# Optimization experiments

Hardware: AMD Instinct MI355X
Metric: run time of the kernel (lower is better)

## Reference

```python
import jax, jax.numpy as jnp
import numpy as np

B, S_SRC, S_TGT, H, C = 32, 128, 129, 512, 32000


def setup_inputs() -> dict:
    key = jax.random.key(0)
    ks = jax.random.split(key, 16)
    sc = 0.02
    return {
        "source": jax.random.randint(ks[0], (B, S_SRC), 0, C),
        "target": jax.random.randint(ks[1], (B, S_TGT), 0, C),
        "embed": jax.random.normal(ks[2], (C, H), jnp.float32) * sc,
        "enc_Wih": jax.random.normal(ks[3], (H, H), jnp.float32) * sc,
        "enc_Whh": jax.random.normal(ks[4], (H, H), jnp.float32) * sc,
        "enc_bih": jnp.zeros((H,), jnp.float32),
        "enc_bhh": jnp.zeros((H,), jnp.float32),
        "dec_Wih": jax.random.normal(ks[5], (H, H), jnp.float32) * sc,
        "dec_Whh": jax.random.normal(ks[6], (H, H), jnp.float32) * sc,
        "dec_bih": jnp.zeros((H,), jnp.float32),
        "dec_bhh": jnp.zeros((H,), jnp.float32),
        "attn_W": jax.random.normal(ks[7], (H, H), jnp.float32) * sc,
        "attn_b": jnp.zeros((H,), jnp.float32),
        "out_W": jax.random.normal(ks[8], (C, 2 * H), jnp.float32) * sc,
        "out_b": jnp.zeros((C,), jnp.float32),
    }


def _rnn(xs, h0, Wih, Whh, bih, bhh):
    # xs: [T, B, H], h0: [B, H]; Elman RNN with tanh (torch nn.RNN default)
    def step(h, x):
        h = jnp.tanh(x @ Wih.T + bih + h @ Whh.T + bhh)
        return h, h
    _, ys = jax.lax.scan(step, h0, xs)
    return ys  # [T, B, H]


def reference(source, target, embed, enc_Wih, enc_Whh, enc_bih, enc_bhh,
              dec_Wih, dec_Whh, dec_bih, dec_bhh, attn_W, attn_b, out_W, out_b):
    dec_input = target[:, :-1]                       # [B, T]
    enc_emb = embed[source].transpose(1, 0, 2)       # [S, B, H]
    dec_emb = embed[dec_input].transpose(1, 0, 2)    # [T, B, H]

    h0 = jnp.zeros((source.shape[0], embed.shape[1]), embed.dtype)
    enc_outputs = _rnn(enc_emb, h0, enc_Wih, enc_Whh, enc_bih, enc_bhh)  # [S, B, H]

    enc_bsh = enc_outputs.transpose(1, 0, 2)                  # [B, S, H]
    enc_t = enc_bsh @ attn_W.T + attn_b                       # [B, S, H] (attn linear)

    def dec_step(h, x):
        h = jnp.tanh(x @ dec_Wih.T + dec_bih + h @ dec_Whh.T + dec_bhh)  # [B, H]
        score = jnp.einsum('bh,bsh->bs', h, enc_t)            # [B, S]
        attn = jax.nn.softmax(score, axis=-1)                 # [B, S]
        ctx = jnp.einsum('bs,bsh->bh', attn, enc_bsh)         # [B, H]
        return h, (jnp.concatenate([h, ctx], axis=-1), attn)

    h_enc = enc_outputs[-1]                                   # [B, H]
    _, (model_hidden, attn_all) = jax.lax.scan(dec_step, h_enc, dec_emb)
    # model_hidden: [T, B, 2H], attn_all: [T, B, S]

    logits = model_hidden @ out_W.T + out_b                   # [T, B, C]
    output_logit = logits.transpose(1, 0, 2)                  # [B, T, C]
    att_weight = attn_all.transpose(1, 2, 0)                  # [B, S, T] = trained_attn.transpose(2,1)
    return output_logit, att_weight
```

## Files before the change

### kernel.cpp

```cpp
#include <hip/hip_runtime.h>
#include <hip/hip_bf16.h>
#include <stdint.h>

typedef unsigned short u16;
typedef __bf16 bf16x8 __attribute__((ext_vector_type(8)));
typedef float f32x4 __attribute__((ext_vector_type(4)));

__device__ __forceinline__ u16 f2bf(float f) {
  uint32_t u = __float_as_uint(f);
  u = (u + 0x7FFFu + ((u >> 16) & 1u)) >> 16;
  return (u16)u;
}

__device__ __forceinline__ void gl2lds16(const void* g, void* l) {
  __builtin_amdgcn_global_load_lds(
      (const __attribute__((address_space(1))) void*)g,
      (__attribute__((address_space(3))) void*)l, 16, 0, 0);
}

__global__ void cvt_bf16_arr(const float* __restrict__ in, u16* __restrict__ out, int n4) {
  int i = blockIdx.x * blockDim.x + threadIdx.x;
  if (i >= n4) return;
  float4 v = ((const float4*)in)[i];
  ushort4 o;
  o.x = f2bf(v.x); o.y = f2bf(v.y); o.z = f2bf(v.z); o.w = f2bf(v.w);
  ((ushort4*)out)[i] = o;
}

__global__ void pack_whh(const float* __restrict__ W, uint32_t* __restrict__ out) {
  int idx = blockIdx.x * 256 + threadIdx.x;
  int p = idx >> 9, j = idx & 511;
  float a = W[j * 512 + 2 * p];
  float b = W[j * 512 + 2 * p + 1];
  out[p * 512 + j] = (uint32_t)f2bf(a) | ((uint32_t)f2bf(b) << 16);
}

__global__ void gather_embed(const int* __restrict__ tok, const float* __restrict__ embed,
                             u16* __restrict__ out, int tokStride) {
  int m = blockIdx.x;
  int t = threadIdx.x;
  int token = tok[(m >> 7) * tokStride + (m & 127)];
  float4 v = ((const float4*)(embed + (long)token * 512))[t];
  ushort4 o;
  o.x = f2bf(v.x); o.y = f2bf(v.y); o.z = f2bf(v.z); o.w = f2bf(v.w);
  ((ushort4*)(out + (long)m * 512))[t] = o;
}

__global__ __launch_bounds__(256) void gemm_bf16_kernel(
    const u16* __restrict__ A, const u16* __restrict__ B,
    const float* __restrict__ bias, float* __restrict__ C,
    int M, int N, int K) {
  __shared__ __align__(16) u16 As[4096];
  __shared__ __align__(16) u16 Bs[4096];
  const int tid = threadIdx.x;
  const int lane = tid & 63;
  const int wv = tid >> 6;
  const int wr = wv >> 1, wc = wv & 1;
  const long m0 = (long)blockIdx.y * 128;
  const long n0 = (long)blockIdx.x * 128;

  f32x4 zero = {0.f, 0.f, 0.f, 0.f};
  f32x4 acc[4][4];
#pragma unroll
  for (int i = 0; i < 4; ++i)
#pragma unroll
    for (int j = 0; j < 4; ++j) acc[i][j] = zero;

  const u16* Ag = A + (m0 + (tid >> 2)) * (long)K + (tid & 3) * 8;
  const u16* Bg = B + (n0 + (tid >> 2)) * (long)K + (tid & 3) * 8;
  const u16* Ag2 = Ag + 64 * (long)K;
  const u16* Bg2 = Bg + 64 * (long)K;
  u16* AsW = As + (tid >> 6) * 512;
  u16* BsW = Bs + (tid >> 6) * 512;
  const int ra = (wr * 64 + (lane & 15)) * 32 + (lane >> 4) * 8;
  const int rb = (wc * 64 + (lane & 15)) * 32 + (lane >> 4) * 8;

  for (int kt = 0; kt < K; kt += 32) {
    __syncthreads();
    gl2lds16(Ag + kt, AsW);
    gl2lds16(Ag2 + kt, AsW + 2048);
    gl2lds16(Bg + kt, BsW);
    gl2lds16(Bg2 + kt, BsW + 2048);
    __syncthreads();
    bf16x8 af[4], bfr[4];
#pragma unroll
    for (int i = 0; i < 4; ++i) af[i] = *(const bf16x8*)&As[ra + i * 512];
#pragma unroll
    for (int j = 0; j < 4; ++j) bfr[j] = *(const bf16x8*)&Bs[rb + j * 512];
#pragma unroll
    for (int i = 0; i < 4; ++i)
#pragma unroll
      for (int j = 0; j < 4; ++j)
        acc[i][j] = __builtin_amdgcn_mfma_f32_16x16x32_bf16(af[i], bfr[j], acc[i][j], 0, 0, 0);
  }

#pragma unroll
  for (int i = 0; i < 4; ++i) {
    const long row = m0 + wr * 64 + i * 16 + ((lane >> 4) << 2);
#pragma unroll
    for (int j = 0; j < 4; ++j) {
      const long col = n0 + wc * 64 + j * 16 + (lane & 15);
      const float bv = bias ? bias[col] : 0.f;
#pragma unroll
      for (int r = 0; r < 4; ++r)
        C[(row + r) * (long)N + col] = acc[i][j][r] + bv;
    }
  }
}

__global__ __launch_bounds__(1024) void enc_rnn(
    const float* __restrict__ pre, const uint32_t* __restrict__ WhhP,
    const float* __restrict__ bih, const float* __restrict__ bhh,
    float* __restrict__ enc_bsh, u16* __restrict__ enc_bf) {
  const int b = blockIdx.x, tid = threadIdx.x;
  const int j = tid & 511, half = tid >> 9;
  __shared__ float h_sh[512];
  __shared__ float part[2][512];
  if (tid < 512) h_sh[tid] = 0.f;
  const float biasj = bih[j] + bhh[j];
  const uint32_t* wp = WhhP + (long)half * 128 * 512 + j;
  const float2* hp = (const float2*)&h_sh[half * 256];
  __syncthreads();
  for (int t = 0; t < 128; ++t) {
    float a0 = 0.f, a1 = 0.f;
#pragma unroll 8
    for (int kk = 0; kk < 128; kk += 2) {
      uint32_t w0 = wp[(long)kk * 512];
      uint32_t w1 = wp[(long)(kk + 1) * 512];
      float2 h0 = hp[kk];
      float2 h1 = hp[kk + 1];
      a0 += h0.x * __uint_as_float(w0 << 16) + h0.y * __uint_as_float(w0 & 0xFFFF0000u);
      a1 += h1.x * __uint_as_float(w1 << 16) + h1.y * __uint_as_float(w1 & 0xFFFF0000u);
    }
    part[half][j] = a0 + a1;
    __syncthreads();
    if (tid < 512) {
      float v = pre[((long)b * 128 + t) * 512 + j] + biasj + part[0][j] + part[1][j];
      float h = tanhf(v);
      h_sh[j] = h;
      enc_bsh[((long)b * 128 + t) * 512 + j] = h;
      enc_bf[((long)b * 128 + t) * 512 + j] = f2bf(h);
    }
    __syncthreads();
  }
}

__global__ __launch_bounds__(1024) void dec_rnn(
    const float* __restrict__ pre, const uint32_t* __restrict__ WhhP,
    const float* __restrict__ bih, const float* __restrict__ bhh,
    const float* __restrict__ enc_t, const float* __restrict__ enc_bsh,
    u16* __restrict__ Hcat, float* __restrict__ att_out) {
  const int b = blockIdx.x, tid = threadIdx.x;
  const int j = tid & 511, half = tid >> 9;
  const int lane = tid & 63, wv = tid >> 6;
  __shared__ float h_sh[512];
  __shared__ float part[2][512];
  __shared__ float sc_sh[128];
  __shared__ float at_sh[128];
  if (tid < 512) h_sh[tid] = enc_bsh[((long)b * 128 + 127) * 512 + tid];
  const float biasj = bih[j] + bhh[j];
  const uint32_t* wp = WhhP + (long)half * 128 * 512 + j;
  const float2* hp = (const float2*)&h_sh[half * 256];
  const float* et_b = enc_t + (long)b * 128 * 512;
  const float* eb_b = enc_bsh + (long)b * 128 * 512;
  __syncthreads();
  for (int t = 0; t < 128; ++t) {
    float a0 = 0.f, a1 = 0.f;
#pragma unroll 8
    for (int kk = 0; kk < 128; kk += 2) {
      uint32_t w0 = wp[(long)kk * 512];
      uint32_t w1 = wp[(long)(kk + 1) * 512];
      float2 h0 = hp[kk];
      float2 h1 = hp[kk + 1];
      a0 += h0.x * __uint_as_float(w0 << 16) + h0.y * __uint_as_float(w0 & 0xFFFF0000u);
      a1 += h1.x * __uint_as_float(w1 << 16) + h1.y * __uint_as_float(w1 & 0xFFFF0000u);
    }
    part[half][j] = a0 + a1;
    __syncthreads();
    float hreg = 0.f;
    if (tid < 512) {
      float v = pre[((long)b * 128 + t) * 512 + j] + biasj + part[0][j] + part[1][j];
      hreg = tanhf(v);
      h_sh[j] = hreg;
    }
    __syncthreads();
#pragma unroll
    for (int q = 0; q < 8; ++q) {
      int s = wv * 8 + q;
      const float* row = et_b + (long)s * 512;
      float a = 0.f;
#pragma unroll
      for (int i = 0; i < 8; ++i) a += h_sh[lane + i * 64] * row[lane + i * 64];
#pragma unroll
      for (int off = 32; off; off >>= 1) a += __shfl_xor(a, off, 64);
      if (lane == 0) sc_sh[s] = a;
    }
    __syncthreads();
    if (tid < 64) {
      float s0 = sc_sh[tid], s1 = sc_sh[tid + 64];
      float mx = fmaxf(s0, s1);
#pragma unroll
      for (int off = 32; off; off >>= 1) mx = fmaxf(mx, __shfl_xor(mx, off, 64));
      float e0 = __expf(s0 - mx), e1 = __expf(s1 - mx);
      float sm = e0 + e1;
#pragma unroll
      for (int off = 32; off; off >>= 1) sm += __shfl_xor(sm, off, 64);
      float inv = 1.f / sm;
      at_sh[tid] = e0 * inv;
      at_sh[tid + 64] = e1 * inv;
    }
    __syncthreads();
    if (tid < 128) att_out[(long)b * 16384 + (long)tid * 128 + t] = at_sh[tid];
    float cacc = 0.f;
#pragma unroll 4
    for (int si = 0; si < 64; ++si) {
      int s = half * 64 + si;
      cacc += at_sh[s] * eb_b[(long)s * 512 + j];
    }
    __syncthreads();
    part[half][j] = cacc;
    __syncthreads();
    if (tid < 512) {
      float ctx = part[0][j] + part[1][j];
      long r = ((long)b * 128 + t) * 1024;
      Hcat[r + j] = f2bf(hreg);
      Hcat[r + 512 + j] = f2bf(ctx);
    }
    __syncthreads();
  }
}

extern "C" void kernel_launch(void* const* d_in, const int* in_sizes, int n_in,
                              void* d_out, int out_size, void* d_ws, size_t ws_size,
                              hipStream_t stream) {
  (void)in_sizes; (void)n_in; (void)out_size; (void)ws_size;
  const int*   source = (const int*)d_in[0];
  const int*   target = (const int*)d_in[1];
  const float* embed  = (const float*)d_in[2];
  const float* encWih = (const float*)d_in[3];
  const float* encWhh = (const float*)d_in[4];
  const float* encBih = (const float*)d_in[5];
  const float* encBhh = (const float*)d_in[6];
  const float* decWih = (const float*)d_in[7];
  const float* decWhh = (const float*)d_in[8];
  const float* decBih = (const float*)d_in[9];
  const float* decBhh = (const float*)d_in[10];
  const float* attnW  = (const float*)d_in[11];
  const float* attnB  = (const float*)d_in[12];
  const float* outW   = (const float*)d_in[13];
  const float* outB   = (const float*)d_in[14];

  float* out_logits = (float*)d_out;
  float* out_att = out_logits + (long)32 * 128 * 32000;

  char* wsb = (char*)d_ws;
  size_t off = 0;
  auto alloc = [&](size_t bytes) {
    char* p = wsb + off;
    off += (bytes + 255) & ~(size_t)255;
    return p;
  };
  u16*      encA   = (u16*)alloc(4096l * 512 * 2);
  u16*      decA   = (u16*)alloc(4096l * 512 * 2);
  u16*      wihE   = (u16*)alloc(512l * 512 * 2);
  u16*      wihD   = (u16*)alloc(512l * 512 * 2);
  u16*      attnWb = (u16*)alloc(512l * 512 * 2);
  uint32_t* whhPe  = (uint32_t*)alloc(256l * 512 * 4);
  uint32_t* whhPd  = (uint32_t*)alloc(256l * 512 * 4);
  u16*      outWb  = (u16*)alloc(32000l * 1024 * 2);
  float*    preE   = (float*)alloc(4096l * 512 * 4);
  float*    preD   = (float*)alloc(4096l * 512 * 4);
  float*    encBsh = (float*)alloc(4096l * 512 * 4);
  u16*      encBf  = (u16*)alloc(4096l * 512 * 2);
  float*    encT   = (float*)alloc(4096l * 512 * 4);
  u16*      hcat   = (u16*)alloc(4096l * 1024 * 2);

  cvt_bf16_arr<<<256, 256, 0, stream>>>(encWih, wihE, 65536);
  cvt_bf16_arr<<<256, 256, 0, stream>>>(decWih, wihD, 65536);
  cvt_bf16_arr<<<256, 256, 0, stream>>>(attnW, attnWb, 65536);
  cvt_bf16_arr<<<32000, 256, 0, stream>>>(outW, outWb, 8192000);
  pack_whh<<<512, 256, 0, stream>>>(encWhh, whhPe);
  pack_whh<<<512, 256, 0, stream>>>(decWhh, whhPd);
  gather_embed<<<4096, 128, 0, stream>>>(source, embed, encA, 128);
  gather_embed<<<4096, 128, 0, stream>>>(target, embed, decA, 129);
  gemm_bf16_kernel<<<dim3(4, 32), 256, 0, stream>>>(encA, wihE, (const float*)nullptr, preE, 4096, 512, 512);
  gemm_bf16_kernel<<<dim3(4, 32), 256, 0, stream>>>(decA, wihD, (const float*)nullptr, preD, 4096, 512, 512);
  enc_rnn<<<32, 1024, 0, stream>>>(preE, whhPe, encBih, encBhh, encBsh, encBf);
  gemm_bf16_kernel<<<dim3(4, 32), 256, 0, stream>>>(encBf, attnWb, attnB, encT, 4096, 512, 512);
  dec_rnn<<<32, 1024, 0, stream>>>(preD, whhPd, decBih, decBhh, encT, encBsh, hcat, out_att);
  gemm_bf16_kernel<<<dim3(250, 32), 256, 0, stream>>>(hcat, outWb, outB, out_logits, 4096, 32000, 1024);
}
```

Measured before the change: 3.177 ms.

## Hoist decoder attention out of the recurrence and keep recurrent weights on-chip

The decoder's attention (scores, softmax, context) does not feed back into the hidden state, so it moves out of the sequential loop into a separate kernel. That kernel processes all 128 timesteps in parallel across a (batch, time-block) grid. A shared rnn_core kernel now serves both encoder and decoder with 512 threads. Each thread keeps 192 packed bf16 weight words in registers and the remaining 64 in LDS, instead of re-reading Whh from global memory every step, and the two-half partial-sum reduction is gone. The risks are register spilling from the large per-thread weight array, and attention now being computed from bf16-rounded hidden states.

```diff
diff --git a/kernel.cpp b/kernel.cpp
--- a/kernel.cpp
+++ b/kernel.cpp
@@ -11,6 +11,11 @@
   u = (u + 0x7FFFu + ((u >> 16) & 1u)) >> 16;
   return (u16)u;
 }
+__device__ __forceinline__ float bf2f(u16 x) {
+  return __uint_as_float(((uint32_t)x) << 16);
+}
+__device__ __forceinline__ float blo(uint32_t w) { return __uint_as_float(w << 16); }
+__device__ __forceinline__ float bhi(uint32_t w) { return __uint_as_float(w & 0xFFFF0000u); }
 
 __device__ __forceinline__ void gl2lds16(const void* g, void* l) {
   __builtin_amdgcn_global_load_lds(
@@ -108,126 +113,120 @@
   }
 }
 
-__global__ __launch_bounds__(1024) void enc_rnn(
-    const float* __restrict__ pre, const uint32_t* __restrict__ WhhP,
+__global__ __launch_bounds__(512, 2) void rnn_core(
+    const float* __restrict__ pre,
+    const uint32_t* __restrict__ WhhP,
     const float* __restrict__ bih, const float* __restrict__ bhh,
-    float* __restrict__ enc_bsh, u16* __restrict__ enc_bf) {
-  const int b = blockIdx.x, tid = threadIdx.x;
-  const int j = tid & 511, half = tid >> 9;
-  __shared__ float h_sh[512];
-  __shared__ float part[2][512];
-  if (tid < 512) h_sh[tid] = 0.f;
+    const float* __restrict__ h0,
+    float* __restrict__ hOutF, long ldF,
+    u16* __restrict__ hOutB, long ldB_,
+    float* __restrict__ hLast)
+{
+  const int b = blockIdx.x, j = threadIdx.x;
+  __shared__ __align__(16) float h_sh[512];
+  __shared__ uint32_t wlds[64][512];
+  uint32_t wreg[192];
+#pragma unroll
+  for (int r = 0; r < 192; ++r) wreg[r] = WhhP[(long)r * 512 + j];
+#pragma unroll
+  for (int p = 0; p < 64; ++p) wlds[p][j] = WhhP[(long)(192 + p) * 512 + j];
   const float biasj = bih[j] + bhh[j];
-  const uint32_t* wp = WhhP + (long)half * 128 * 512 + j;
-  const float2* hp = (const float2*)&h_sh[half * 256];
+  h_sh[j] = h0 ? h0[(long)b * 512 + j] : 0.f;
+  const float* preB = pre + (long)b * 128 * 512 + j;
   __syncthreads();
+
   for (int t = 0; t < 128; ++t) {
-    float a0 = 0.f, a1 = 0.f;
-#pragma unroll 8
-    for (int kk = 0; kk < 128; kk += 2) {
-      uint32_t w0 = wp[(long)kk * 512];
-      uint32_t w1 = wp[(long)(kk + 1) * 512];
-      float2 h0 = hp[kk];
-      float2 h1 = hp[kk + 1];
-      a0 += h0.x * __uint_as_float(w0 << 16) + h0.y * __uint_as_float(w0 & 0xFFFF0000u);
-      a1 += h1.x * __uint_as_float(w1 << 16) + h1.y * __uint_as_float(w1 & 0xFFFF0000u);
+    const float4* H4 = (const float4*)h_sh;
+    float a0 = 0.f, a1 = 0.f, a2 = 0.f, a3 = 0.f;
+#pragma unroll
+    for (int g = 0; g < 48; ++g) {
+      float4 ha = H4[2 * g];
+      float4 hb = H4[2 * g + 1];
+      uint32_t w0 = wreg[4 * g], w1 = wreg[4 * g + 1];
+      uint32_t w2 = wreg[4 * g + 2], w3 = wreg[4 * g + 3];
+      a0 += ha.x * blo(w0) + ha.y * bhi(w0);
+      a1 += ha.z * blo(w1) + ha.w * bhi(w1);
+      a2 += hb.x * blo(w2) + hb.y * bhi(w2);
+      a3 += hb.z * blo(w3) + hb.w * bhi(w3);
     }
-    part[half][j] = a0 + a1;
-    __syncthreads();
-    if (tid < 512) {
-      float v = pre[((long)b * 128 + t) * 512 + j] + biasj + part[0][j] + part[1][j];
-      float h = tanhf(v);
-      h_sh[j] = h;
-      enc_bsh[((long)b * 128 + t) * 512 + j] = h;
-      enc_bf[((long)b * 128 + t) * 512 + j] = f2bf(h);
+#pragma unroll
+    for (int g = 0; g < 16; ++g) {
+      float4 ha = H4[96 + 2 * g];
+      float4 hb = H4[96 + 2 * g + 1];
+      uint32_t w0 = wlds[4 * g][j], w1 = wlds[4 * g + 1][j];
+      uint32_t w2 = wlds[4 * g + 2][j], w3 = wlds[4 * g + 3][j];
+      a0 += ha.x * blo(w0) + ha.y * bhi(w0);
+      a1 += ha.z * blo(w1) + ha.w * bhi(w1);
+      a2 += hb.x * blo(w2) + hb.y * bhi(w2);
+      a3 += hb.z * blo(w3) + hb.w * bhi(w3);
     }
-    __syncthreads();
-  }
-}
-
-__global__ __launch_bounds__(1024) void dec_rnn(
-    const float* __restrict__ pre, const uint32_t* __restrict__ WhhP,
-    const float* __restrict__ bih, const float* __restrict__ bhh,
-    const float* __restrict__ enc_t, const float* __restrict__ enc_bsh,
-    u16* __restrict__ Hcat, float* __restrict__ att_out) {
-  const int b = blockIdx.x, tid = threadIdx.x;
-  const int j = tid & 511, half = tid >> 9;
-  const int lane = tid & 63, wv = tid >> 6;
-  __shared__ float h_sh[512];
-  __shared__ float part[2][512];
-  __shared__ float sc_sh[128];
-  __shared__ float at_sh[128];
-  if (tid < 512) h_sh[tid] = enc_bsh[((long)b * 128 + 127) * 512 + tid];
-  const float biasj = bih[j] + bhh[j];
-  const uint32_t* wp = WhhP + (long)half * 128 * 512 + j;
-  const float2* hp = (const float2*)&h_sh[half * 256];
-  const float* et_b = enc_t + (long)b * 128 * 512;
-  const float* eb_b = enc_bsh + (long)b * 128 * 512;
+    float h = tanhf(preB[(long)t * 512] + biasj + ((a0 + a1) + (a2 + a3)));
+    __syncthreads();
+    h_sh[j] = h;
+    if (hOutF) hOutF[((long)b * 128 + t) * ldF + j] = h;
+    hOutB[((long)b * 128 + t) * ldB_ + j] = f2bf(h);
+    if (hLast && t == 127) hLast[(long)b * 512 + j] = h;
+    __syncthreads();
+  }
+}
+
+__global__ __launch_bounds__(1024) void attn_fused(
+    const u16* __restrict__ hcat,
+    const float* __restrict__ encT,
+    const float* __restrict__ encBsh,
+    u16* __restrict__ hcatW,
+    float* __restrict__ attOut)
+{
+  const int b = blockIdx.x;
+  const int w = threadIdx.x >> 6, lane = threadIdx.x & 63;
+  const int t = blockIdx.y * 16 + w;
+  __shared__ float at[16][128];
+
+  float hreg[8];
+  const u16* hrow = hcat + ((long)b * 128 + t) * 1024;
+#pragma unroll
+  for (int i = 0; i < 8; ++i) hreg[i] = bf2f(hrow[lane + i * 64]);
+
+  const float* et = encT + (long)b * 128 * 512;
+  for (int s = 0; s < 128; ++s) {
+    const float* row = et + (long)s * 512;
+    float a = 0.f;
+#pragma unroll
+    for (int i = 0; i < 8; ++i) a += hreg[i] * row[lane + i * 64];
+#pragma unroll
+    for (int o = 32; o; o >>= 1) a += __shfl_xor(a, o, 64);
+    if (lane == 0) at[w][s] = a;
+  }
   __syncthreads();
-  for (int t = 0; t < 128; ++t) {
-    float a0 = 0.f, a1 = 0.f;
-#pragma unroll 8
-    for (int kk = 0; kk < 128; kk += 2) {
-      uint32_t w0 = wp[(long)kk * 512];
-      uint32_t w1 = wp[(long)(kk + 1) * 512];
-      float2 h0 = hp[kk];
-      float2 h1 = hp[kk + 1];
-      a0 += h0.x * __uint_as_float(w0 << 16) + h0.y * __uint_as_float(w0 & 0xFFFF0000u);
-      a1 += h1.x * __uint_as_float(w1 << 16) + h1.y * __uint_as_float(w1 & 0xFFFF0000u);
-    }
-    part[half][j] = a0 + a1;
-    __syncthreads();
-    float hreg = 0.f;
-    if (tid < 512) {
-      float v = pre[((long)b * 128 + t) * 512 + j] + biasj + part[0][j] + part[1][j];
-      hreg = tanhf(v);
-      h_sh[j] = hreg;
-    }
-    __syncthreads();
-#pragma unroll
-    for (int q = 0; q < 8; ++q) {
-      int s = wv * 8 + q;
-      const float* row = et_b + (long)s * 512;
-      float a = 0.f;
-#pragma unroll
-      for (int i = 0; i < 8; ++i) a += h_sh[lane + i * 64] * row[lane + i * 64];
-#pragma unroll
-      for (int off = 32; off; off >>= 1) a += __shfl_xor(a, off, 64);
-      if (lane == 0) sc_sh[s] = a;
-    }
-    __syncthreads();
-    if (tid < 64) {
-      float s0 = sc_sh[tid], s1 = sc_sh[tid + 64];
-      float mx = fmaxf(s0, s1);
-#pragma unroll
-      for (int off = 32; off; off >>= 1) mx = fmaxf(mx, __shfl_xor(mx, off, 64));
-      float e0 = __expf(s0 - mx), e1 = __expf(s1 - mx);
-      float sm = e0 + e1;
-#pragma unroll
-      for (int off = 32; off; off >>= 1) sm += __shfl_xor(sm, off, 64);
-      float inv = 1.f / sm;
-      at_sh[tid] = e0 * inv;
-      at_sh[tid + 64] = e1 * inv;
-    }
-    __syncthreads();
-    if (tid < 128) att_out[(long)b * 16384 + (long)tid * 128 + t] = at_sh[tid];
-    float cacc = 0.f;
-#pragma unroll 4
-    for (int si = 0; si < 64; ++si) {
-      int s = half * 64 + si;
-      cacc += at_sh[s] * eb_b[(long)s * 512 + j];
-    }
-    __syncthreads();
-    part[half][j] = cacc;
-    __syncthreads();
-    if (tid < 512) {
-      float ctx = part[0][j] + part[1][j];
-      long r = ((long)b * 128 + t) * 1024;
-      Hcat[r + j] = f2bf(hreg);
-      Hcat[r + 512 + j] = f2bf(ctx);
-    }
-    __syncthreads();
-  }
+
+  float s0 = at[w][lane], s1 = at[w][lane + 64];
+  float mx = fmaxf(s0, s1);
+#pragma unroll
+  for (int o = 32; o; o >>= 1) mx = fmaxf(mx, __shfl_xor(mx, o, 64));
+  float e0 = __expf(s0 - mx), e1 = __expf(s1 - mx);
+  float sm = e0 + e1;
+#pragma unroll
+  for (int o = 32; o; o >>= 1) sm += __shfl_xor(sm, o, 64);
+  float inv = 1.f / sm;
+  e0 *= inv; e1 *= inv;
+  at[w][lane] = e0;
+  at[w][lane + 64] = e1;
+  __syncthreads();
+
+  attOut[(long)b * 16384 + (long)lane * 128 + t] = e0;
+  attOut[(long)b * 16384 + (long)(lane + 64) * 128 + t] = e1;
+
+  float acc[8] = {0.f, 0.f, 0.f, 0.f, 0.f, 0.f, 0.f, 0.f};
+  const float* eb = encBsh + (long)b * 128 * 512;
+  for (int s = 0; s < 128; ++s) {
+    float ws = at[w][s];
+    const float* row = eb + (long)s * 512;
+#pragma unroll
+    for (int i = 0; i < 8; ++i) acc[i] += ws * row[lane + i * 64];
+  }
+  u16* crow = hcatW + ((long)b * 128 + t) * 1024 + 512;
+#pragma unroll
+  for (int i = 0; i < 8; ++i) crow[lane + i * 64] = f2bf(acc[i]);
 }
 
 extern "C" void kernel_launch(void* const* d_in, const int* in_sizes, int n_in,
@@ -273,6 +272,7 @@
   float*    encBsh = (float*)alloc(4096l * 512 * 4);
   u16*      encBf  = (u16*)alloc(4096l * 512 * 2);
   float*    encT   = (float*)alloc(4096l * 512 * 4);
+  float*    hlast  = (float*)alloc(32l * 512 * 4);
   u16*      hcat   = (u16*)alloc(4096l * 1024 * 2);
 
   cvt_bf16_arr<<<256, 256, 0, stream>>>(encWih, wihE, 65536);
@@ -285,8 +285,11 @@
   gather_embed<<<4096, 128, 0, stream>>>(target, embed, decA, 129);
   gemm_bf16_kernel<<<dim3(4, 32), 256, 0, stream>>>(encA, wihE, (const float*)nullptr, preE, 4096, 512, 512);
   gemm_bf16_kernel<<<dim3(4, 32), 256, 0, stream>>>(decA, wihD, (const float*)nullptr, preD, 4096, 512, 512);
-  enc_rnn<<<32, 1024, 0, stream>>>(preE, whhPe, encBih, encBhh, encBsh, encBf);
+  rnn_core<<<32, 512, 0, stream>>>(preE, whhPe, encBih, encBhh,
+      (const float*)nullptr, encBsh, 512, encBf, 512, hlast);
   gemm_bf16_kernel<<<dim3(4, 32), 256, 0, stream>>>(encBf, attnWb, attnB, encT, 4096, 512, 512);
-  dec_rnn<<<32, 1024, 0, stream>>>(preD, whhPd, decBih, decBhh, encT, encBsh, hcat, out_att);
+  rnn_core<<<32, 512, 0, stream>>>(preD, whhPd, decBih, decBhh,
+      hlast, (float*)nullptr, 512, hcat, 1024, (float*)nullptr);
+  attn_fused<<<dim3(32, 8), 1024, 0, stream>>>(hcat, encT, encBsh, hcat, out_att);
   gemm_bf16_kernel<<<dim3(250, 32), 256, 0, stream>>>(hcat, outWb, outB, out_logits, 4096, 32000, 1024);
 }
```

Result: slower. 5.021 ms (+58.0%).
